# Performance work log

Measured on AMD Instinct MI355X. Metric: run time of the kernel, lower is better.

## Reference

```python
import jax, jax.numpy as jnp
import numpy as np

EPS = 1e-8        # LinearGELU eps
LN_EPS = 1e-5     # LayerNorm eps
NUM_HEADS = 16
DIM = 1024
HIDDEN = 4096
B, N = 4, 785


def _lin(x, xj, w, lw, b=None, lb=None):
    # LinearLinear: primal linear + JVP wrt input and tangent params (lw, lb)
    y = x @ w.T
    yj = xj @ w.T + x @ lw.T
    if b is not None:
        y = y + b
    if lb is not None:
        yj = yj + lb
    return y, yj


def _ln(x, xj, w, b, lw, lb):
    # LinearLayerNorm forward + manual JVP (matches torch source exactly)
    mean = x.mean(-1, keepdims=True)
    xc = x - mean
    var = (xc * xc).mean(-1, keepdims=True)
    std = jnp.sqrt(var + LN_EPS)
    xhat = xc / std
    out = xhat * w + b
    t1 = xhat * lw + lb                              # tangent wrt affine params
    mj = xj.mean(-1, keepdims=True)
    xjc = xj - mj
    a = xjc * std
    corr = 2.0 * (xc * xjc).mean(-1, keepdims=True)
    bterm = (0.5 / std) * corr * xc
    c = (1.0 / std) ** 2 * (a - bterm)
    return out, t1 + c * w


def _gelu(x, xj):
    # exact (erf) GELU; jvp uses gelu(x)/(x+EPS) + x*pdf(x) as in source
    out = 0.5 * x * (1.0 + jax.lax.erf(x * np.float32(1.0 / np.sqrt(2.0))))
    pdf = jnp.exp(-0.5 * x * x) * np.float32(1.0 / np.sqrt(2.0 * np.pi))
    return out, xj * (out / (x + EPS) + x * pdf)


def _attn(x, xj, qkv_w, qkv_lw, proj_w, proj_b, proj_lw, proj_lb):
    Bb, Nn, C = x.shape
    H = NUM_HEADS
    D = C // H
    scale = np.float32(D) ** -0.5
    qkv, qkv_j = _lin(x, xj, qkv_w, qkv_lw)  # [B,N,3C], qkv_bias=False
    def split(t):
        return t.reshape(Bb, Nn, 3, H, D).transpose(2, 0, 3, 1, 4)
    q, k, v = split(qkv)
    qj, kj, vj = split(qkv_j)
    q = q * scale
    qj = qj * scale
    attn = jax.nn.softmax(jnp.einsum('bhnd,bhmd->bhnm', q, k), axis=-1)
    out = jnp.einsum('bhnm,bhmd->bhnd', attn, v)
    # softmax JVP: dm = A_jvp + B_jvp; filter = dm*attn - rowsum(dm*attn)*attn
    dm = jnp.einsum('bhnd,bhmd->bhnm', qj, k) + jnp.einsum('bhnd,bhmd->bhnm', q, kj)
    f = dm * attn
    filt = f - f.sum(-1, keepdims=True) * attn  # == diag(dm @ attn^T) * attn correction
    out_j = jnp.einsum('bhnm,bhmd->bhnd', filt, v) + jnp.einsum('bhnm,bhmd->bhnd', attn, vj)
    out = out.transpose(0, 2, 1, 3).reshape(Bb, Nn, C)
    out_j = out_j.transpose(0, 2, 1, 3).reshape(Bb, Nn, C)
    return _lin(out, out_j, proj_w, proj_lw, proj_b, proj_lb)


def setup_inputs() -> dict:
    keys = jax.random.split(jax.random.key(0), 32)
    ki = iter(keys)
    def nrm(shape, s=0.02):
        return (jax.random.normal(next(ki), shape, jnp.float32) * s).astype(jnp.float32)
    d, h = DIM, HIDDEN
    inp = {
        'input': jax.random.normal(next(ki), (B, N, d), jnp.float32),
        'input_jvp': jax.random.normal(next(ki), (B, N, d), jnp.float32),
        'n1_w': 1.0 + nrm((d,), 0.1), 'n1_b': nrm((d,), 0.1),
        'n1_lw': nrm((d,), 0.1), 'n1_lb': nrm((d,), 0.1),
        'qkv_w': nrm((3 * d, d)), 'qkv_lw': nrm((3 * d, d)),
        'proj_w': nrm((d, d)), 'proj_b': nrm((d,), 0.1),
        'proj_lw': nrm((d, d)), 'proj_lb': nrm((d,), 0.1),
        'n2_w': 1.0 + nrm((d,), 0.1), 'n2_b': nrm((d,), 0.1),
        'n2_lw': nrm((d,), 0.1), 'n2_lb': nrm((d,), 0.1),
        'fc1_w': nrm((h, d)), 'fc1_b': nrm((h,), 0.1),
        'fc1_lw': nrm((h, d)), 'fc1_lb': nrm((h,), 0.1),
        'fc2_w': nrm((d, h)), 'fc2_b': nrm((d,), 0.1),
        'fc2_lw': nrm((d, h)), 'fc2_lb': nrm((d,), 0.1),
    }
    return inp


def reference(input, input_jvp, n1_w, n1_b, n1_lw, n1_lb, qkv_w, qkv_lw,
              proj_w, proj_b, proj_lw, proj_lb, n2_w, n2_b, n2_lw, n2_lb,
              fc1_w, fc1_b, fc1_lw, fc1_lb, fc2_w, fc2_b, fc2_lw, fc2_lb):
    x, xj = _ln(input, input_jvp, n1_w, n1_b, n1_lw, n1_lb)
    x, xj = _attn(x, xj, qkv_w, qkv_lw, proj_w, proj_b, proj_lw, proj_lb)
    x = x + input
    xj = xj + input_jvp
    i2, i2j = x, xj
    x, xj = _ln(x, xj, n2_w, n2_b, n2_lw, n2_lb)
    x, xj = _lin(x, xj, fc1_w, fc1_lw, fc1_b, fc1_lb)
    x, xj = _gelu(x, xj)
    x, xj = _lin(x, xj, fc2_w, fc2_lw, fc2_b, fc2_lb)
    return (x + i2, xj + i2j)
```

## Files before the change

kernel.cpp:

```cpp
#include <hip/hip_runtime.h>
#include <hip/hip_bf16.h>

typedef unsigned short u16;
typedef unsigned int   u32;

#define MP     3328
#define MREAL  3140
#define DIMC   1024
#define H3C    3072
#define HIDC   4096
#define NKV    785
#define SLEN   896

typedef __bf16 bf16x8 __attribute__((ext_vector_type(8)));
typedef float  f32x4  __attribute__((ext_vector_type(4)));

#define MFMA(d,a,b) (d) = __builtin_amdgcn_mfma_f32_16x16x32_bf16((a),(b),(d),0,0,0)

__device__ __forceinline__ u16 f2bf(float f){
  u32 u = __builtin_bit_cast(u32, f);
  return (u16)((u + 0x7fffu + ((u >> 16) & 1u)) >> 16);
}
__device__ __forceinline__ float bf2f(u16 h){
  return __builtin_bit_cast(float, (u32)h << 16);
}
__device__ __forceinline__ void gload16(const u16* g, u16* l){
  __builtin_amdgcn_global_load_lds(
      (const __attribute__((address_space(1))) void*)g,
      (__attribute__((address_space(3))) void*)l, 16, 0, 0);
}
__device__ __forceinline__ float wsum(float v){
  #pragma unroll
  for (int o = 32; o >= 1; o >>= 1) v += __shfl_xor(v, o);
  return v;
}

__global__ __launch_bounds__(256) void cvt_k(const float* __restrict__ in,
                                             u16* __restrict__ out, int n){
  int i = (blockIdx.x * 256 + threadIdx.x) * 4;
  if (i >= n) return;
  float4 v = *(const float4*)(in + i);
  ushort4 o4;
  o4.x = f2bf(v.x); o4.y = f2bf(v.y); o4.z = f2bf(v.z); o4.w = f2bf(v.w);
  *(ushort4*)(out + i) = o4;
}

__global__ __launch_bounds__(256) void ln_jvp_k(
    const float* __restrict__ x, const float* __restrict__ xj,
    const float* __restrict__ w, const float* __restrict__ b,
    const float* __restrict__ lw, const float* __restrict__ lb,
    u16* __restrict__ out, u16* __restrict__ outj)
{
  const int row = blockIdx.x, t = threadIdx.x;
  const size_t ro = (size_t)row * DIMC;
  if (row >= MREAL){
    for (int i = t; i < DIMC; i += 256){ out[ro+i] = 0; outj[ro+i] = 0; }
    return;
  }
  const float4 v  = ((const float4*)(x  + ro))[t];
  const float4 vj = ((const float4*)(xj + ro))[t];
  float sx  = v.x+v.y+v.z+v.w;
  float sxx = v.x*v.x+v.y*v.y+v.z*v.z+v.w*v.w;
  float sj  = vj.x+vj.y+vj.z+vj.w;
  float sxj = v.x*vj.x+v.y*vj.y+v.z*vj.z+v.w*vj.w;
  __shared__ __attribute__((aligned(64))) float red[4][4];
  sx = wsum(sx); sxx = wsum(sxx); sj = wsum(sj); sxj = wsum(sxj);
  const int wid = t>>6, lane = t&63;
  if (lane == 0){ red[wid][0]=sx; red[wid][1]=sxx; red[wid][2]=sj; red[wid][3]=sxj; }
  __syncthreads();
  sx  = red[0][0]+red[1][0]+red[2][0]+red[3][0];
  sxx = red[0][1]+red[1][1]+red[2][1]+red[3][1];
  sj  = red[0][2]+red[1][2]+red[2][2]+red[3][2];
  sxj = red[0][3]+red[1][3]+red[2][3]+red[3][3];
  const float inv  = 1.0f/1024.0f;
  const float mean = sx*inv, meanj = sj*inv;
  const float var  = sxx*inv - mean*mean;
  const float cov  = sxj*inv - mean*meanj;
  const float rstd = rsqrtf(var + 1e-5f);
  const float r3   = rstd*rstd*rstd;
  const float4 wv  = ((const float4*)w)[t];
  const float4 bv  = ((const float4*)b)[t];
  const float4 lwv = ((const float4*)lw)[t];
  const float4 lbv = ((const float4*)lb)[t];
  const float xs[4]  = {v.x,v.y,v.z,v.w},   xjs[4] = {vj.x,vj.y,vj.z,vj.w};
  const float wss[4] = {wv.x,wv.y,wv.z,wv.w}, bs[4] = {bv.x,bv.y,bv.z,bv.w};
  const float lws[4] = {lwv.x,lwv.y,lwv.z,lwv.w}, lbs[4] = {lbv.x,lbv.y,lbv.z,lbv.w};
  const int i0 = t*4;
  #pragma unroll
  for (int e = 0; e < 4; e++){
    const float xc = xs[e]-mean, xjc = xjs[e]-meanj;
    const float xhat = xc*rstd;
    const float cc = xjc*rstd - xc*cov*r3;
    out [ro+i0+e] = f2bf(xhat*wss[e] + bs[e]);
    outj[ro+i0+e] = f2bf(xhat*lws[e] + lbs[e] + cc*wss[e]);
  }
}

template<int EPI>
__global__ __launch_bounds__(256) void gemm_jvp_k(
    const u16* __restrict__ A, const u16* __restrict__ Aj, int lda,
    const u16* __restrict__ B, const u16* __restrict__ Bj, int K,
    const float* __restrict__ bias, const float* __restrict__ biasj,
    const float* __restrict__ res, const float* __restrict__ resj,
    void* __restrict__ Yv, void* __restrict__ Yjv, int ldy, int mwrite)
{
  __shared__ __attribute__((aligned(128))) u16 lds[2][4][128*32];
  const int tid = threadIdx.x, wid = tid>>6, lane = tid&63;
  const int m0 = blockIdx.y*128, n0 = blockIdx.x*128;
  f32x4 accY[4][4], accJ[4][4];
  #pragma unroll
  for (int i = 0; i < 4; i++)
    #pragma unroll
    for (int j = 0; j < 4; j++){
      accY[i][j] = (f32x4){0.f,0.f,0.f,0.f};
      accJ[i][j] = (f32x4){0.f,0.f,0.f,0.f};
    }
  const int bo0 = wid*1024 + lane*16;
  const int bo1 = bo0 + 4096;
  const int sb0 = bo0 ^ (((bo0>>7)&7)<<4);
  const int sb1 = bo1 ^ (((bo1>>7)&7)<<4);
  const int r0 = sb0>>6, c0 = (sb0&63)>>1;
  const int r1 = sb1>>6, c1 = (sb1&63)>>1;
  const u16* A0  = A  + (size_t)(m0+r0)*lda + c0;
  const u16* A1  = A  + (size_t)(m0+r1)*lda + c1;
  const u16* Aj0 = Aj + (size_t)(m0+r0)*lda + c0;
  const u16* Aj1 = Aj + (size_t)(m0+r1)*lda + c1;
  const u16* B0  = B  + (size_t)(n0+r0)*K + c0;
  const u16* B1  = B  + (size_t)(n0+r1)*K + c1;
  const u16* Bj0 = Bj + (size_t)(n0+r0)*K + c0;
  const u16* Bj1 = Bj + (size_t)(n0+r1)*K + c1;
  const int kq = (lane>>4)<<3;
  const int ar = (wid>>1)*64 + (lane&15);
  const int bc = (wid&1)*64 + (lane&15);
  int aoff[4], boff[4];
  #pragma unroll
  for (int i = 0; i < 4; i++){
    int ab_ = (ar+i*16)*64 + (kq<<1);
    aoff[i] = ab_ ^ (((ab_>>7)&7)<<4);
    int bb_ = (bc+i*16)*64 + (kq<<1);
    boff[i] = bb_ ^ (((bb_>>7)&7)<<4);
  }
  auto STAGE = [&](int buf, int k0){
    u16* p0 = &lds[buf][0][0];
    gload16(A0 +k0, p0+(bo0>>1)); gload16(A1 +k0, p0+(bo1>>1));
    u16* p1 = &lds[buf][1][0];
    gload16(Aj0+k0, p1+(bo0>>1)); gload16(Aj1+k0, p1+(bo1>>1));
    u16* p2 = &lds[buf][2][0];
    gload16(B0 +k0, p2+(bo0>>1)); gload16(B1 +k0, p2+(bo1>>1));
    u16* p3 = &lds[buf][3][0];
    gload16(Bj0+k0, p3+(bo0>>1)); gload16(Bj1+k0, p3+(bo1>>1));
  };
  const int nt = K >> 5;
  STAGE(0, 0);
  __syncthreads();
  int cur = 0;
  for (int t = 0; t < nt; t++){
    if (t + 1 < nt) STAGE(cur^1, (t+1)<<5);
    const char* lAb  = (const char*)&lds[cur][0][0];
    const char* lAjb = (const char*)&lds[cur][1][0];
    const char* lBb  = (const char*)&lds[cur][2][0];
    const char* lBjb = (const char*)&lds[cur][3][0];
    bf16x8 af[4], ajf[4], bbf[4], bjf[4];
    #pragma unroll
    for (int i = 0; i < 4; i++){
      af[i]  = *(const bf16x8*)(lAb  + aoff[i]);
      ajf[i] = *(const bf16x8*)(lAjb + aoff[i]);
      bbf[i] = *(const bf16x8*)(lBb  + boff[i]);
      bjf[i] = *(const bf16x8*)(lBjb + boff[i]);
    }
    __builtin_amdgcn_s_setprio(1);
    #pragma unroll
    for (int i = 0; i < 4; i++)
      #pragma unroll
      for (int j = 0; j < 4; j++){
        MFMA(accY[i][j], af[i],  bbf[j]);
        MFMA(accJ[i][j], ajf[i], bbf[j]);
        MFMA(accJ[i][j], af[i],  bjf[j]);
      }
    __builtin_amdgcn_s_setprio(0);
    __syncthreads();
    cur ^= 1;
  }
  const int mb = m0 + (wid>>1)*64 + ((lane>>4)<<2);
  const int nb = n0 + (wid&1)*64 + (lane&15);
  #pragma unroll
  for (int i = 0; i < 4; i++)
    #pragma unroll
    for (int j = 0; j < 4; j++)
      #pragma unroll
      for (int r = 0; r < 4; r++){
        const int m = mb + i*16 + r, n = nb + j*16;
        float y = accY[i][j][r], yj = accJ[i][j][r];
        if (EPI == 0){
          ((u16*)Yv )[(size_t)m*ldy+n] = f2bf(y);
          ((u16*)Yjv)[(size_t)m*ldy+n] = f2bf(yj);
        } else if (EPI == 1){
          if (m < mwrite){
            y  += bias[n]  + res [(size_t)m*ldy+n];
            yj += biasj[n] + resj[(size_t)m*ldy+n];
            ((float*)Yv )[(size_t)m*ldy+n] = y;
            ((float*)Yjv)[(size_t)m*ldy+n] = yj;
          }
        } else {
          y  += bias[n];
          yj += biasj[n];
          const float ge  = 0.5f*y*(1.0f + erff(y*0.70710678118654752f));
          const float pdf = expf(-0.5f*y*y)*0.3989422804014327f;
          const float gj  = yj*(ge/(y + 1e-8f) + y*pdf);
          ((u16*)Yv )[(size_t)m*ldy+n] = f2bf(ge);
          ((u16*)Yjv)[(size_t)m*ldy+n] = f2bf(gj);
        }
      }
}

__global__ __launch_bounds__(256) void transpose_v_k(
    const u16* __restrict__ qkvb, const u16* __restrict__ qkvjb,
    u16* __restrict__ vT, u16* __restrict__ vjT)
{
  __shared__ __attribute__((aligned(64))) u16 tl[64][80];
  __shared__ __attribute__((aligned(64))) u16 tlj[64][80];
  const int kt = blockIdx.x, bh = blockIdx.y;
  const int b = bh>>4, h = bh&15;
  const int t = threadIdx.x;
  const int kv = t>>2, dd = (t&3)*16;
  const int kvg = kt*64 + kv;
  if (kvg < NKV){
    const u16* s0 = qkvb  + (size_t)(b*NKV+kvg)*H3C + 2048 + h*64 + dd;
    const u16* s1 = qkvjb + (size_t)(b*NKV+kvg)*H3C + 2048 + h*64 + dd;
    *(uint4*)&tl [kv][dd]   = *(const uint4*)s0;
    *(uint4*)&tl [kv][dd+8] = *(const uint4*)(s0+8);
    *(uint4*)&tlj[kv][dd]   = *(const uint4*)s1;
    *(uint4*)&tlj[kv][dd+8] = *(const uint4*)(s1+8);
  } else {
    uint4 z = {0,0,0,0};
    *(uint4*)&tl [kv][dd] = z; *(uint4*)&tl [kv][dd+8] = z;
    *(uint4*)&tlj[kv][dd] = z; *(uint4*)&tlj[kv][dd+8] = z;
  }
  __syncthreads();
  const int d = t>>2, kc = (t&3)*16;
  u16* d0 = vT  + ((size_t)bh*64 + d)*SLEN + kt*64 + kc;
  u16* d1 = vjT + ((size_t)bh*64 + d)*SLEN + kt*64 + kc;
  #pragma unroll
  for (int e = 0; e < 16; e++){ d0[e] = tl[kc+e][d]; d1[e] = tlj[kc+e][d]; }
}

__global__ __launch_bounds__(256) void flash_attn_jvp_k(
    const u16* __restrict__ qkvb, const u16* __restrict__ qkvjb,
    const u16* __restrict__ vT, const u16* __restrict__ vjT,
    u16* __restrict__ o, u16* __restrict__ oj)
{
  __shared__ __attribute__((aligned(64))) u16 lK  [64*64];
  __shared__ __attribute__((aligned(64))) u16 lKj [64*64];
  __shared__ __attribute__((aligned(64))) u16 lvT [64*64];
  __shared__ __attribute__((aligned(64))) u16 lvjT[64*64];
  __shared__ __attribute__((aligned(64))) u16 pl  [128*64];
  __shared__ __attribute__((aligned(64))) u16 pdl [128*64];
  const int tid = threadIdx.x, wid = tid>>6, lane = tid&63;
  const int l4 = lane>>4, l15 = lane&15;
  const int qt = blockIdx.x, bh = blockIdx.y, b = bh>>4, h = bh&15;

  bf16x8 qf[2][2], qjf[2][2];
  {
    const size_t qrb = (size_t)b*NKV + qt*128 + wid*32;
    #pragma unroll
    for (int i = 0; i < 2; i++){
      const size_t ro = (qrb + i*16 + l15)*H3C + h*64;
      #pragma unroll
      for (int ks = 0; ks < 2; ks++){
        qf [i][ks] = *(const bf16x8*)(qkvb  + ro + ks*32 + l4*8);
        qjf[i][ks] = *(const bf16x8*)(qkvjb + ro + ks*32 + l4*8);
      }
    }
  }
  float m_st[2][4], l_st[2][4], g_st[2][4];
  f32x4 PO[2][4], PTJ[2][4];
  #pragma unroll
  for (int i = 0; i < 2; i++)
    #pragma unroll
    for (int r = 0; r < 4; r++){
      m_st[i][r] = -1e30f; l_st[i][r] = 0.f; g_st[i][r] = 0.f;
    }
  #pragma unroll
  for (int i = 0; i < 2; i++)
    #pragma unroll
    for (int j = 0; j < 4; j++){
      PO[i][j] = (f32x4){0.f,0.f,0.f,0.f};
      PTJ[i][j] = (f32x4){0.f,0.f,0.f,0.f};
    }
  const char* lKb   = (const char*)lK;
  const char* lKjb  = (const char*)lKj;
  const char* lvTb  = (const char*)lvT;
  const char* lvjTb = (const char*)lvjT;
  char* plb  = (char*)pl;
  char* pdlb = (char*)pdl;

  for (int t = 0; t < 13; t++){
    #pragma unroll
    for (int rnd = 0; rnd < 2; rnd++){
      const int gidx = rnd*256 + tid;
      const int row = gidx>>3, c = gidx&7;
      const int cs = c ^ (row&7);
      const size_t ksrc = (size_t)(b*NKV + t*64 + row)*H3C + 1024 + h*64 + cs*8;
      gload16(qkvb  + ksrc, lK  + gidx*8);
      gload16(qkvjb + ksrc, lKj + gidx*8);
      const size_t vsrc = ((size_t)bh*64 + row)*SLEN + t*64 + cs*8;
      gload16(vT  + vsrc, lvT  + gidx*8);
      gload16(vjT + vsrc, lvjT + gidx*8);
    }
    __syncthreads();

    #pragma unroll
    for (int i = 0; i < 2; i++){
      f32x4 s[4], dm[4];
      #pragma unroll
      for (int j = 0; j < 4; j++){
        s[j] = (f32x4){0.f,0.f,0.f,0.f};
        dm[j] = (f32x4){0.f,0.f,0.f,0.f};
      }
      #pragma unroll
      for (int ks = 0; ks < 2; ks++){
        #pragma unroll
        for (int j = 0; j < 4; j++){
          const int row = j*16 + l15;
          const int byt = (row*128 + ks*64 + l4*16) ^ ((row&7)<<4);
          const bf16x8 kf  = *(const bf16x8*)(lKb  + byt);
          const bf16x8 kjf = *(const bf16x8*)(lKjb + byt);
          MFMA(s[j],  qf[i][ks],  kf);
          MFMA(dm[j], qjf[i][ks], kf);
          MFMA(dm[j], qf[i][ks],  kjf);
        }
      }
      float tm[4] = {-1e30f,-1e30f,-1e30f,-1e30f};
      #pragma unroll
      for (int j = 0; j < 4; j++){
        const int colg = t*64 + j*16 + l15;
        #pragma unroll
        for (int r = 0; r < 4; r++){
          float sv = s[j][r]*0.125f;
          if (colg >= NKV) sv = -1e30f;
          s[j][r] = sv;
          dm[j][r] *= 0.125f;
          tm[r] = fmaxf(tm[r], sv);
        }
      }
      #pragma unroll
      for (int r = 0; r < 4; r++){
        float v = tm[r];
        v = fmaxf(v, __shfl_xor(v, 1));
        v = fmaxf(v, __shfl_xor(v, 2));
        v = fmaxf(v, __shfl_xor(v, 4));
        v = fmaxf(v, __shfl_xor(v, 8));
        const float mn = fmaxf(m_st[i][r], v);
        const float sc = __expf(m_st[i][r] - mn);
        m_st[i][r] = mn;
        l_st[i][r] *= sc;
        g_st[i][r] *= sc;
        #pragma unroll
        for (int j = 0; j < 4; j++){ PO[i][j][r] *= sc; PTJ[i][j][r] *= sc; }
      }
      float ps[4] = {0.f,0.f,0.f,0.f}, pds[4] = {0.f,0.f,0.f,0.f};
      #pragma unroll
      for (int j = 0; j < 4; j++){
        const int col = j*16 + l15;
        #pragma unroll
        for (int r = 0; r < 4; r++){
          const float p  = __expf(s[j][r] - m_st[i][r]);
          const float pd = p * dm[j][r];
          ps[r] += p; pds[r] += pd;
          const int row = wid*32 + i*16 + l4*4 + r;
          const int byt = (row*128 + col*2) ^ ((row&7)<<4);
          *(u16*)(plb  + byt) = f2bf(p);
          *(u16*)(pdlb + byt) = f2bf(pd);
        }
      }
      #pragma unroll
      for (int r = 0; r < 4; r++){
        float v = ps[r], w = pds[r];
        v += __shfl_xor(v, 1); w += __shfl_xor(w, 1);
        v += __shfl_xor(v, 2); w += __shfl_xor(w, 2);
        v += __shfl_xor(v, 4); w += __shfl_xor(w, 4);
        v += __shfl_xor(v, 8); w += __shfl_xor(w, 8);
        l_st[i][r] += v; g_st[i][r] += w;
      }
    }

    #pragma unroll
    for (int ks = 0; ks < 2; ks++){
      bf16x8 pa[2], pda[2];
      #pragma unroll
      for (int i = 0; i < 2; i++){
        const int row = wid*32 + i*16 + l15;
        const int byt = (row*128 + ks*64 + l4*16) ^ ((row&7)<<4);
        pa[i]  = *(const bf16x8*)(plb  + byt);
        pda[i] = *(const bf16x8*)(pdlb + byt);
      }
      #pragma unroll
      for (int j = 0; j < 4; j++){
        const int row = j*16 + l15;
        const int byt = (row*128 + ks*64 + l4*16) ^ ((row&7)<<4);
        const bf16x8 vb  = *(const bf16x8*)(lvTb  + byt);
        const bf16x8 vjb = *(const bf16x8*)(lvjTb + byt);
        #pragma unroll
        for (int i = 0; i < 2; i++){
          MFMA(PO[i][j],  pa[i],  vb);
          MFMA(PTJ[i][j], pda[i], vb);
          MFMA(PTJ[i][j], pa[i],  vjb);
        }
      }
    }
    __syncthreads();
  }

  #pragma unroll
  for (int i = 0; i < 2; i++)
    #pragma unroll
    for (int r = 0; r < 4; r++){
      const int ql = qt*128 + wid*32 + i*16 + l4*4 + r;
      if (ql < NKV){
        const float rl = 1.0f / l_st[i][r];
        const float gg = g_st[i][r] * rl;
        #pragma unroll
        for (int j = 0; j < 4; j++){
          const size_t oo = ((size_t)b*NKV + ql)*DIMC + h*64 + j*16 + l15;
          const float po = PO[i][j][r] * rl;
          o [oo] = f2bf(po);
          oj[oo] = f2bf(PTJ[i][j][r]*rl - gg*po);
        }
      }
    }
}

extern "C" void kernel_launch(void* const* d_in, const int* in_sizes, int n_in,
                              void* d_out, int out_size, void* d_ws, size_t ws_size,
                              hipStream_t stream)
{
  (void)in_sizes; (void)n_in; (void)out_size;
  const float* input   = (const float*)d_in[0];
  const float* inputj  = (const float*)d_in[1];
  const float* n1_w    = (const float*)d_in[2];
  const float* n1_b    = (const float*)d_in[3];
  const float* n1_lw   = (const float*)d_in[4];
  const float* n1_lb   = (const float*)d_in[5];
  const float* qkv_w   = (const float*)d_in[6];
  const float* qkv_lw  = (const float*)d_in[7];
  const float* proj_w  = (const float*)d_in[8];
  const float* proj_b  = (const float*)d_in[9];
  const float* proj_lw = (const float*)d_in[10];
  const float* proj_lb = (const float*)d_in[11];
  const float* n2_w    = (const float*)d_in[12];
  const float* n2_b    = (const float*)d_in[13];
  const float* n2_lw   = (const float*)d_in[14];
  const float* n2_lb   = (const float*)d_in[15];
  const float* fc1_w   = (const float*)d_in[16];
  const float* fc1_b   = (const float*)d_in[17];
  const float* fc1_lw  = (const float*)d_in[18];
  const float* fc1_lb  = (const float*)d_in[19];
  const float* fc2_w   = (const float*)d_in[20];
  const float* fc2_b   = (const float*)d_in[21];
  const float* fc2_lw  = (const float*)d_in[22];
  const float* fc2_lb  = (const float*)d_in[23];

  const size_t SZ_W      = 2u*4194304u*2u;
  const size_t SZ_ARENA1 = 2u*(size_t)MP*HIDC*2u;
  const size_t SZ_VT     = (size_t)64*64*SLEN*2u;
  const size_t SZ_ARENA2 = 2u*SZ_VT;
  const size_t SZ_ARENA3 = 2u*(size_t)MP*DIMC*2u;
  const size_t SZ_X2     = (size_t)MP*DIMC*4u;
  const size_t NEEDED = SZ_W + SZ_ARENA1 + SZ_ARENA2 + SZ_ARENA3 + 2u*SZ_X2 + 4096u;
  if (ws_size < NEEDED) return;

  char* base = (char*)d_ws;
  size_t off = 0;
  auto ab = [&](size_t bytes)->char*{
    char* p = base + off;
    off += bytes; off = (off + 255) & ~(size_t)255;
    return p;
  };
  char* Wslot  = ab(SZ_W);
  char* arena1 = ab(SZ_ARENA1);
  char* arena2 = ab(SZ_ARENA2);
  char* arena3 = ab(SZ_ARENA3);
  float* x2  = (float*)ab(SZ_X2);
  float* x2j = (float*)ab(SZ_X2);

  u16* wbuf  = (u16*)Wslot;
  u16* wjbuf = wbuf + 4194304;
  u16* qkvb  = (u16*)arena1;
  u16* qkvjb = qkvb + (size_t)MP*H3C;
  u16* hb    = (u16*)arena1;
  u16* hjb   = hb + (size_t)MP*HIDC;
  u16* vT    = (u16*)arena2;
  u16* vjT   = vT + (size_t)64*64*SLEN;
  u16* x3b   = (u16*)arena2;
  u16* x3jb  = x3b + (size_t)MP*DIMC;
  u16* x1b   = (u16*)arena3;
  u16* x1jb  = x1b + (size_t)MP*DIMC;
  u16* ob    = (u16*)arena3;
  u16* ojb   = ob + (size_t)MP*DIMC;

  auto cvt = [&](const float* src, u16* dst, int n){
    cvt_k<<<dim3((n + 1023)/1024), 256, 0, stream>>>(src, dst, n);
  };

  ln_jvp_k<<<dim3(MP), 256, 0, stream>>>(input, inputj, n1_w, n1_b, n1_lw, n1_lb,
                                         x1b, x1jb);
  cvt(qkv_w, wbuf, H3C*DIMC); cvt(qkv_lw, wjbuf, H3C*DIMC);
  gemm_jvp_k<0><<<dim3(H3C/128, MP/128), 256, 0, stream>>>(
      x1b, x1jb, DIMC, wbuf, wjbuf, DIMC, nullptr, nullptr, nullptr, nullptr,
      qkvb, qkvjb, H3C, MP);
  transpose_v_k<<<dim3(14, 64), 256, 0, stream>>>(qkvb, qkvjb, vT, vjT);
  flash_attn_jvp_k<<<dim3(7, 64), 256, 0, stream>>>(qkvb, qkvjb, vT, vjT, ob, ojb);
  cvt(proj_w, wbuf, DIMC*DIMC); cvt(proj_lw, wjbuf, DIMC*DIMC);
  gemm_jvp_k<1><<<dim3(DIMC/128, MP/128), 256, 0, stream>>>(
      ob, ojb, DIMC, wbuf, wjbuf, DIMC, proj_b, proj_lb, input, inputj,
      x2, x2j, DIMC, MREAL);
  ln_jvp_k<<<dim3(MP), 256, 0, stream>>>(x2, x2j, n2_w, n2_b, n2_lw, n2_lb,
                                         x3b, x3jb);
  cvt(fc1_w, wbuf, HIDC*DIMC); cvt(fc1_lw, wjbuf, HIDC*DIMC);
  gemm_jvp_k<2><<<dim3(HIDC/128, MP/128), 256, 0, stream>>>(
      x3b, x3jb, DIMC, wbuf, wjbuf, DIMC, fc1_b, fc1_lb, nullptr, nullptr,
      hb, hjb, HIDC, MP);
  cvt(fc2_w, wbuf, DIMC*HIDC); cvt(fc2_lw, wjbuf, DIMC*HIDC);
  float* out0 = (float*)d_out;
  float* out1 = out0 + (size_t)MREAL*DIMC;
  gemm_jvp_k<1><<<dim3(DIMC/128, MP/128), 256, 0, stream>>>(
      hb, hjb, HIDC, wbuf, wjbuf, HIDC, fc2_b, fc2_lb, x2, x2j,
      out0, out1, DIMC, MREAL);
}
```

Measured before the change: 633.0 us.

## Add 256x128 triple-buffered 512-thread GEMM for QKV and FC1 JVP

Introduces a wider GEMM kernel with 256-row M tiles, 8 waves per block and a three-stage LDS ring. It is used for the QKV and FC1 projections, so each B weight tile is reused across twice as many rows and loads can be issued two stages ahead. The GELU epilogue also switches expf to the faster __expf intrinsic. The trade-off is more LDS per block (about 144 KB) and fewer blocks per grid, which may cut occupancy and leave a bigger tail on the GPU.

Result: faster. 572.4 us (-9.6%).

```diff
diff --git a/kernel.cpp b/kernel.cpp
--- a/kernel.cpp
+++ b/kernel.cpp
@@ -97,6 +97,112 @@
 }
 
 template<int EPI>
+__global__ __launch_bounds__(512, 2) void gemm_jvp_wide_k(
+    const u16* __restrict__ A, const u16* __restrict__ Aj, int lda,
+    const u16* __restrict__ B, const u16* __restrict__ Bj, int K,
+    const float* __restrict__ bias, const float* __restrict__ biasj,
+    void* __restrict__ Yv, void* __restrict__ Yjv, int ldy)
+{
+  __shared__ __attribute__((aligned(128))) u16 lds[3][24576];
+  const int tid = threadIdx.x, wid = tid>>6, lane = tid&63;
+  const int l4 = lane>>4, l15 = lane&15;
+  const int m0 = blockIdx.y*256, n0 = blockIdx.x*128;
+  f32x4 accY[4][4], accJ[4][4];
+  #pragma unroll
+  for (int i = 0; i < 4; i++)
+    #pragma unroll
+    for (int j = 0; j < 4; j++){
+      accY[i][j] = (f32x4){0.f,0.f,0.f,0.f};
+      accJ[i][j] = (f32x4){0.f,0.f,0.f,0.f};
+    }
+  const int boA0 = tid*16,        boA1 = (512+tid)*16;
+  const int sbA0 = boA0 ^ (((boA0>>7)&7)<<4);
+  const int sbA1 = boA1 ^ (((boA1>>7)&7)<<4);
+  const int rA0 = sbA0>>6, cA0 = (sbA0&63)>>1;
+  const int rA1 = sbA1>>6, cA1 = (sbA1&63)>>1;
+  const int boB = tid*16;
+  const int sbB = boB ^ (((boB>>7)&7)<<4);
+  const int rB = sbB>>6, cB = (sbB&63)>>1;
+  const u16* srcA0  = A  + (size_t)(m0+rA0)*lda + cA0;
+  const u16* srcA1  = A  + (size_t)(m0+rA1)*lda + cA1;
+  const u16* srcAj0 = Aj + (size_t)(m0+rA0)*lda + cA0;
+  const u16* srcAj1 = Aj + (size_t)(m0+rA1)*lda + cA1;
+  const u16* srcB   = B  + (size_t)(n0+rB)*K + cB;
+  const u16* srcBj  = Bj + (size_t)(n0+rB)*K + cB;
+  const int dA0 = tid*8, dA1 = (512+tid)*8, dB = tid*8;
+  const int wr = wid>>1, wc = wid&1;
+  int aoff[4], boff[4];
+  #pragma unroll
+  for (int i = 0; i < 4; i++){
+    int ab_ = (wr*64 + i*16 + l15)*64 + l4*16;
+    aoff[i] = ab_ ^ (((ab_>>7)&7)<<4);
+    int bb_ = (wc*64 + i*16 + l15)*64 + l4*16;
+    boff[i] = bb_ ^ (((bb_>>7)&7)<<4);
+  }
+  auto STAGE = [&](int buf, int t){
+    const int k0 = t<<5;
+    u16* Lb = &lds[buf][0];
+    gload16(srcA0 +k0, Lb + dA0);
+    gload16(srcA1 +k0, Lb + dA1);
+    gload16(srcAj0+k0, Lb + 8192 + dA0);
+    gload16(srcAj1+k0, Lb + 8192 + dA1);
+    gload16(srcB  +k0, Lb + 16384 + dB);
+    gload16(srcBj +k0, Lb + 20480 + dB);
+  };
+  const int nt = K >> 5;
+  STAGE(0, 0);
+  STAGE(1, 1);
+  for (int t = 0; t < nt; t++){
+    if (t + 1 < nt) asm volatile("s_waitcnt vmcnt(6)" ::: "memory");
+    else            asm volatile("s_waitcnt vmcnt(0)" ::: "memory");
+    __builtin_amdgcn_s_barrier();
+    if (t + 2 < nt) STAGE((t+2)%3, t+2);
+    const char* Lb = (const char*)&lds[t%3][0];
+    bf16x8 af[4], ajf[4], bbf[4], bjf[4];
+    #pragma unroll
+    for (int i = 0; i < 4; i++){
+      af[i]  = *(const bf16x8*)(Lb + aoff[i]);
+      ajf[i] = *(const bf16x8*)(Lb + 16384 + aoff[i]);
+      bbf[i] = *(const bf16x8*)(Lb + 32768 + boff[i]);
+      bjf[i] = *(const bf16x8*)(Lb + 40960 + boff[i]);
+    }
+    __builtin_amdgcn_s_setprio(1);
+    #pragma unroll
+    for (int i = 0; i < 4; i++)
+      #pragma unroll
+      for (int j = 0; j < 4; j++){
+        MFMA(accY[i][j], af[i],  bbf[j]);
+        MFMA(accJ[i][j], ajf[i], bbf[j]);
+        MFMA(accJ[i][j], af[i],  bjf[j]);
+      }
+    __builtin_amdgcn_s_setprio(0);
+  }
+  const int mb = m0 + wr*64 + (l4<<2);
+  const int nb = n0 + wc*64 + l15;
+  #pragma unroll
+  for (int i = 0; i < 4; i++)
+    #pragma unroll
+    for (int j = 0; j < 4; j++)
+      #pragma unroll
+      for (int r = 0; r < 4; r++){
+        const int m = mb + i*16 + r, n = nb + j*16;
+        float y = accY[i][j][r], yj = accJ[i][j][r];
+        if (EPI == 0){
+          ((u16*)Yv )[(size_t)m*ldy+n] = f2bf(y);
+          ((u16*)Yjv)[(size_t)m*ldy+n] = f2bf(yj);
+        } else {
+          y  += bias[n];
+          yj += biasj[n];
+          const float ge  = 0.5f*y*(1.0f + erff(y*0.70710678118654752f));
+          const float pdf = __expf(-0.5f*y*y)*0.3989422804014327f;
+          const float gj  = yj*(ge/(y + 1e-8f) + y*pdf);
+          ((u16*)Yv )[(size_t)m*ldy+n] = f2bf(ge);
+          ((u16*)Yjv)[(size_t)m*ldy+n] = f2bf(gj);
+        }
+      }
+}
+
+template<int EPI>
 __global__ __launch_bounds__(256) void gemm_jvp_k(
     const u16* __restrict__ A, const u16* __restrict__ Aj, int lda,
     const u16* __restrict__ B, const u16* __restrict__ Bj, int K,
@@ -205,7 +311,7 @@
           y  += bias[n];
           yj += biasj[n];
           const float ge  = 0.5f*y*(1.0f + erff(y*0.70710678118654752f));
-          const float pdf = expf(-0.5f*y*y)*0.3989422804014327f;
+          const float pdf = __expf(-0.5f*y*y)*0.3989422804014327f;
           const float gj  = yj*(ge/(y + 1e-8f) + y*pdf);
           ((u16*)Yv )[(size_t)m*ldy+n] = f2bf(ge);
           ((u16*)Yjv)[(size_t)m*ldy+n] = f2bf(gj);
@@ -505,9 +611,9 @@
   ln_jvp_k<<<dim3(MP), 256, 0, stream>>>(input, inputj, n1_w, n1_b, n1_lw, n1_lb,
                                          x1b, x1jb);
   cvt(qkv_w, wbuf, H3C*DIMC); cvt(qkv_lw, wjbuf, H3C*DIMC);
-  gemm_jvp_k<0><<<dim3(H3C/128, MP/128), 256, 0, stream>>>(
-      x1b, x1jb, DIMC, wbuf, wjbuf, DIMC, nullptr, nullptr, nullptr, nullptr,
-      qkvb, qkvjb, H3C, MP);
+  gemm_jvp_wide_k<0><<<dim3(H3C/128, MP/256), 512, 0, stream>>>(
+      x1b, x1jb, DIMC, wbuf, wjbuf, DIMC, nullptr, nullptr,
+      qkvb, qkvjb, H3C);
   transpose_v_k<<<dim3(14, 64), 256, 0, stream>>>(qkvb, qkvjb, vT, vjT);
   flash_attn_jvp_k<<<dim3(7, 64), 256, 0, stream>>>(qkvb, qkvjb, vT, vjT, ob, ojb);
   cvt(proj_w, wbuf, DIMC*DIMC); cvt(proj_lw, wjbuf, DIMC*DIMC);
@@ -517,9 +623,9 @@
   ln_jvp_k<<<dim3(MP), 256, 0, stream>>>(x2, x2j, n2_w, n2_b, n2_lw, n2_lb,
                                          x3b, x3jb);
   cvt(fc1_w, wbuf, HIDC*DIMC); cvt(fc1_lw, wjbuf, HIDC*DIMC);
-  gemm_jvp_k<2><<<dim3(HIDC/128, MP/128), 256, 0, stream>>>(
-      x3b, x3jb, DIMC, wbuf, wjbuf, DIMC, fc1_b, fc1_lb, nullptr, nullptr,
-      hb, hjb, HIDC, MP);
+  gemm_jvp_wide_k<2><<<dim3(HIDC/128, MP/256), 512, 0, stream>>>(
+      x3b, x3jb, DIMC, wbuf, wjbuf, DIMC, fc1_b, fc1_lb,
+      hb, hjb, HIDC);
   cvt(fc2_w, wbuf, DIMC*HIDC); cvt(fc2_lw, wjbuf, DIMC*HIDC);
   float* out0 = (float*)d_out;
   float* out1 = out0 + (size_t)MREAL*DIMC;
```

## Widen JVP GEMM tiles to 256 rows with 8 waves and triple-buffered LDS

Applied to the files above, without the earlier changes.

The JVP GEMM now uses 512-thread blocks covering a 256x128 output tile, so the B/Bj weight tiles staged in LDS are shared by twice as many A rows. The two-buffer loop with __syncthreads is replaced by a three-stage ring that prefetches two k-steps ahead, using explicit vmcnt waits and a single barrier per iteration. The GELU epilogue also switches to the fast __expf intrinsic. The costs are 144 KB of LDS per block, fewer blocks in the grid (tail effects, with MP=3328 giving 13 row tiles), and reliance on hand-counted vmcnt values being correct.

New measurement: 604.4 us. 4.5% less time.

```diff
diff --git a/kernel.cpp b/kernel.cpp
--- a/kernel.cpp
+++ b/kernel.cpp
@@ -97,16 +97,17 @@
 }
 
 template<int EPI>
-__global__ __launch_bounds__(256) void gemm_jvp_k(
+__global__ __launch_bounds__(512, 2) void gemm_jvp_wide_k(
     const u16* __restrict__ A, const u16* __restrict__ Aj, int lda,
     const u16* __restrict__ B, const u16* __restrict__ Bj, int K,
     const float* __restrict__ bias, const float* __restrict__ biasj,
     const float* __restrict__ res, const float* __restrict__ resj,
     void* __restrict__ Yv, void* __restrict__ Yjv, int ldy, int mwrite)
 {
-  __shared__ __attribute__((aligned(128))) u16 lds[2][4][128*32];
+  __shared__ __attribute__((aligned(128))) u16 lds[3][24576];
   const int tid = threadIdx.x, wid = tid>>6, lane = tid&63;
-  const int m0 = blockIdx.y*128, n0 = blockIdx.x*128;
+  const int l4 = lane>>4, l15 = lane&15;
+  const int m0 = blockIdx.y*256, n0 = blockIdx.x*128;
   f32x4 accY[4][4], accJ[4][4];
   #pragma unroll
   for (int i = 0; i < 4; i++)
@@ -115,58 +116,56 @@
       accY[i][j] = (f32x4){0.f,0.f,0.f,0.f};
       accJ[i][j] = (f32x4){0.f,0.f,0.f,0.f};
     }
-  const int bo0 = wid*1024 + lane*16;
-  const int bo1 = bo0 + 4096;
-  const int sb0 = bo0 ^ (((bo0>>7)&7)<<4);
-  const int sb1 = bo1 ^ (((bo1>>7)&7)<<4);
-  const int r0 = sb0>>6, c0 = (sb0&63)>>1;
-  const int r1 = sb1>>6, c1 = (sb1&63)>>1;
-  const u16* A0  = A  + (size_t)(m0+r0)*lda + c0;
-  const u16* A1  = A  + (size_t)(m0+r1)*lda + c1;
-  const u16* Aj0 = Aj + (size_t)(m0+r0)*lda + c0;
-  const u16* Aj1 = Aj + (size_t)(m0+r1)*lda + c1;
-  const u16* B0  = B  + (size_t)(n0+r0)*K + c0;
-  const u16* B1  = B  + (size_t)(n0+r1)*K + c1;
-  const u16* Bj0 = Bj + (size_t)(n0+r0)*K + c0;
-  const u16* Bj1 = Bj + (size_t)(n0+r1)*K + c1;
-  const int kq = (lane>>4)<<3;
-  const int ar = (wid>>1)*64 + (lane&15);
-  const int bc = (wid&1)*64 + (lane&15);
+  const int boA0 = tid*16,        boA1 = (512+tid)*16;
+  const int sbA0 = boA0 ^ (((boA0>>7)&7)<<4);
+  const int sbA1 = boA1 ^ (((boA1>>7)&7)<<4);
+  const int rA0 = sbA0>>6, cA0 = (sbA0&63)>>1;
+  const int rA1 = sbA1>>6, cA1 = (sbA1&63)>>1;
+  const int boB = tid*16;
+  const int sbB = boB ^ (((boB>>7)&7)<<4);
+  const int rB = sbB>>6, cB = (sbB&63)>>1;
+  const u16* srcA0  = A  + (size_t)(m0+rA0)*lda + cA0;
+  const u16* srcA1  = A  + (size_t)(m0+rA1)*lda + cA1;
+  const u16* srcAj0 = Aj + (size_t)(m0+rA0)*lda + cA0;
+  const u16* srcAj1 = Aj + (size_t)(m0+rA1)*lda + cA1;
+  const u16* srcB   = B  + (size_t)(n0+rB)*K + cB;
+  const u16* srcBj  = Bj + (size_t)(n0+rB)*K + cB;
+  const int dA0 = tid*8, dA1 = (512+tid)*8, dB = tid*8;
+  const int wr = wid>>1, wc = wid&1;
   int aoff[4], boff[4];
   #pragma unroll
   for (int i = 0; i < 4; i++){
-    int ab_ = (ar+i*16)*64 + (kq<<1);
+    int ab_ = (wr*64 + i*16 + l15)*64 + l4*16;
     aoff[i] = ab_ ^ (((ab_>>7)&7)<<4);
-    int bb_ = (bc+i*16)*64 + (kq<<1);
+    int bb_ = (wc*64 + i*16 + l15)*64 + l4*16;
     boff[i] = bb_ ^ (((bb_>>7)&7)<<4);
   }
-  auto STAGE = [&](int buf, int k0){
-    u16* p0 = &lds[buf][0][0];
-    gload16(A0 +k0, p0+(bo0>>1)); gload16(A1 +k0, p0+(bo1>>1));
-    u16* p1 = &lds[buf][1][0];
-    gload16(Aj0+k0, p1+(bo0>>1)); gload16(Aj1+k0, p1+(bo1>>1));
-    u16* p2 = &lds[buf][2][0];
-    gload16(B0 +k0, p2+(bo0>>1)); gload16(B1 +k0, p2+(bo1>>1));
-    u16* p3 = &lds[buf][3][0];
-    gload16(Bj0+k0, p3+(bo0>>1)); gload16(Bj1+k0, p3+(bo1>>1));
+  auto STAGE = [&](int buf, int t){
+    const int k0 = t<<5;
+    u16* Lb = &lds[buf][0];
+    gload16(srcA0 +k0, Lb + dA0);
+    gload16(srcA1 +k0, Lb + dA1);
+    gload16(srcAj0+k0, Lb + 8192 + dA0);
+    gload16(srcAj1+k0, Lb + 8192 + dA1);
+    gload16(srcB  +k0, Lb + 16384 + dB);
+    gload16(srcBj +k0, Lb + 20480 + dB);
   };
   const int nt = K >> 5;
   STAGE(0, 0);
-  __syncthreads();
-  int cur = 0;
+  STAGE(1, 1);
   for (int t = 0; t < nt; t++){
-    if (t + 1 < nt) STAGE(cur^1, (t+1)<<5);
-    const char* lAb  = (const char*)&lds[cur][0][0];
-    const char* lAjb = (const char*)&lds[cur][1][0];
-    const char* lBb  = (const char*)&lds[cur][2][0];
-    const char* lBjb = (const char*)&lds[cur][3][0];
+    if (t + 1 < nt) asm volatile("s_waitcnt vmcnt(6)" ::: "memory");
+    else            asm volatile("s_waitcnt vmcnt(0)" ::: "memory");
+    __builtin_amdgcn_s_barrier();
+    if (t + 2 < nt) STAGE((t+2)%3, t+2);
+    const char* Lb = (const char*)&lds[t%3][0];
     bf16x8 af[4], ajf[4], bbf[4], bjf[4];
     #pragma unroll
     for (int i = 0; i < 4; i++){
-      af[i]  = *(const bf16x8*)(lAb  + aoff[i]);
-      ajf[i] = *(const bf16x8*)(lAjb + aoff[i]);
-      bbf[i] = *(const bf16x8*)(lBb  + boff[i]);
-      bjf[i] = *(const bf16x8*)(lBjb + boff[i]);
+      af[i]  = *(const bf16x8*)(Lb + aoff[i]);
+      ajf[i] = *(const bf16x8*)(Lb + 16384 + aoff[i]);
+      bbf[i] = *(const bf16x8*)(Lb + 32768 + boff[i]);
+      bjf[i] = *(const bf16x8*)(Lb + 40960 + boff[i]);
     }
     __builtin_amdgcn_s_setprio(1);
     #pragma unroll
@@ -178,11 +177,9 @@
         MFMA(accJ[i][j], af[i],  bjf[j]);
       }
     __builtin_amdgcn_s_setprio(0);
-    __syncthreads();
-    cur ^= 1;
-  }
-  const int mb = m0 + (wid>>1)*64 + ((lane>>4)<<2);
-  const int nb = n0 + (wid&1)*64 + (lane&15);
+  }
+  const int mb = m0 + wr*64 + (l4<<2);
+  const int nb = n0 + wc*64 + l15;
   #pragma unroll
   for (int i = 0; i < 4; i++)
     #pragma unroll
@@ -205,7 +202,7 @@
           y  += bias[n];
           yj += biasj[n];
           const float ge  = 0.5f*y*(1.0f + erff(y*0.70710678118654752f));
-          const float pdf = expf(-0.5f*y*y)*0.3989422804014327f;
+          const float pdf = __expf(-0.5f*y*y)*0.3989422804014327f;
           const float gj  = yj*(ge/(y + 1e-8f) + y*pdf);
           ((u16*)Yv )[(size_t)m*ldy+n] = f2bf(ge);
           ((u16*)Yjv)[(size_t)m*ldy+n] = f2bf(gj);
@@ -505,25 +502,25 @@
   ln_jvp_k<<<dim3(MP), 256, 0, stream>>>(input, inputj, n1_w, n1_b, n1_lw, n1_lb,
                                          x1b, x1jb);
   cvt(qkv_w, wbuf, H3C*DIMC); cvt(qkv_lw, wjbuf, H3C*DIMC);
-  gemm_jvp_k<0><<<dim3(H3C/128, MP/128), 256, 0, stream>>>(
+  gemm_jvp_wide_k<0><<<dim3(H3C/128, MP/256), 512, 0, stream>>>(
       x1b, x1jb, DIMC, wbuf, wjbuf, DIMC, nullptr, nullptr, nullptr, nullptr,
       qkvb, qkvjb, H3C, MP);
   transpose_v_k<<<dim3(14, 64), 256, 0, stream>>>(qkvb, qkvjb, vT, vjT);
   flash_attn_jvp_k<<<dim3(7, 64), 256, 0, stream>>>(qkvb, qkvjb, vT, vjT, ob, ojb);
   cvt(proj_w, wbuf, DIMC*DIMC); cvt(proj_lw, wjbuf, DIMC*DIMC);
-  gemm_jvp_k<1><<<dim3(DIMC/128, MP/128), 256, 0, stream>>>(
+  gemm_jvp_wide_k<1><<<dim3(DIMC/128, MP/256), 512, 0, stream>>>(
       ob, ojb, DIMC, wbuf, wjbuf, DIMC, proj_b, proj_lb, input, inputj,
       x2, x2j, DIMC, MREAL);
   ln_jvp_k<<<dim3(MP), 256, 0, stream>>>(x2, x2j, n2_w, n2_b, n2_lw, n2_lb,
                                          x3b, x3jb);
   cvt(fc1_w, wbuf, HIDC*DIMC); cvt(fc1_lw, wjbuf, HIDC*DIMC);
-  gemm_jvp_k<2><<<dim3(HIDC/128, MP/128), 256, 0, stream>>>(
+  gemm_jvp_wide_k<2><<<dim3(HIDC/128, MP/256), 512, 0, stream>>>(
       x3b, x3jb, DIMC, wbuf, wjbuf, DIMC, fc1_b, fc1_lb, nullptr, nullptr,
       hb, hjb, HIDC, MP);
   cvt(fc2_w, wbuf, DIMC*HIDC); cvt(fc2_lw, wjbuf, DIMC*HIDC);
   float* out0 = (float*)d_out;
   float* out1 = out0 + (size_t)MREAL*DIMC;
-  gemm_jvp_k<1><<<dim3(DIMC/128, MP/128), 256, 0, stream>>>(
+  gemm_jvp_wide_k<1><<<dim3(DIMC/128, MP/256), 512, 0, stream>>>(
       hb, hjb, HIDC, wbuf, wjbuf, HIDC, fc2_b, fc2_lb, x2, x2j,
       out0, out1, DIMC, MREAL);
 }
```
